# Optimization experiments

Measured on AMD Instinct MI355X. Metric: run time of the kernel, lower is better.

## Reference

```python
import jax, jax.numpy as jnp
import numpy as np

E = 524288
B = 16
NODE_IN = 128
EDGE_IN = 64
GLOBAL_IN = 64
HIDDEN = 256
EDGE_OUT = 64
CAT_IN = EDGE_IN + 2 * NODE_IN + GLOBAL_IN  # 384


def setup_inputs() -> dict:
    key = jax.random.key(0)
    ks = jax.random.split(key, 9)
    src = jax.random.normal(ks[0], (E, NODE_IN), dtype=jnp.float32)
    dest = jax.random.normal(ks[1], (E, NODE_IN), dtype=jnp.float32)
    edge_attr = jax.random.normal(ks[2], (E, EDGE_IN), dtype=jnp.float32)
    u = jax.random.normal(ks[3], (B, GLOBAL_IN), dtype=jnp.float32)
    batch = jnp.sort(jax.random.randint(ks[4], (E,), 0, B, dtype=jnp.int64))
    # MLP params (torch Linear default init scale ~1/sqrt(fan_in))
    W1 = jax.random.normal(ks[5], (CAT_IN, HIDDEN), dtype=jnp.float32) / np.sqrt(CAT_IN)
    b1 = jax.random.normal(ks[6], (HIDDEN,), dtype=jnp.float32) / np.sqrt(CAT_IN)
    W2 = jax.random.normal(ks[7], (HIDDEN, EDGE_OUT), dtype=jnp.float32) / np.sqrt(HIDDEN)
    b2 = jax.random.normal(ks[8], (EDGE_OUT,), dtype=jnp.float32) / np.sqrt(HIDDEN)
    return {"src": src, "dest": dest, "edge_attr": edge_attr, "u": u,
            "batch": batch, "W1": W1, "b1": b1, "W2": W2, "b2": b2}


def reference(src, dest, edge_attr, u, batch, W1, b1, W2, b2):
    # gather global features per edge, concat, 2-layer MLP with ReLU
    x = jnp.concatenate([src, dest, edge_attr, u[batch]], axis=1)  # [E, 384]
    h = jax.nn.relu(x @ W1 + b1)                                   # [E, hidden]
    return h @ W2 + b2                                             # [E, edge_out]
```

## Files before the change

### kernel.cpp

```cpp
#include <hip/hip_runtime.h>

typedef __bf16 bf16_t;
typedef bf16_t bf16x8 __attribute__((ext_vector_type(8)));
typedef float f32x4 __attribute__((ext_vector_type(4)));
typedef unsigned short u16;
typedef unsigned int u32;

#define E_TOT 524288
#define MT 64
#define NBLK (E_TOT / MT)

__device__ __forceinline__ u16 f2bf(float f) {
  u32 u = __builtin_bit_cast(u32, f);
  u += 0x7FFFu + ((u >> 16) & 1u);
  return (u16)(u >> 16);
}

__device__ __forceinline__ bf16x8 pack8(f32x4 a, f32x4 b) {
  bf16x8 p;
  p[0] = (bf16_t)a[0]; p[1] = (bf16_t)a[1]; p[2] = (bf16_t)a[2]; p[3] = (bf16_t)a[3];
  p[4] = (bf16_t)b[0]; p[5] = (bf16_t)b[1]; p[6] = (bf16_t)b[2]; p[7] = (bf16_t)b[3];
  return p;
}

__device__ __forceinline__ void gload_lds16(const void* g, void* l) {
  __builtin_amdgcn_global_load_lds(
      (const __attribute__((address_space(1))) u32*)g,
      (__attribute__((address_space(3))) u32*)l, 16, 0, 0);
}

__global__ void prep_w1tc(const float* __restrict__ W1, u16* __restrict__ W1Tc) {
  int t = blockIdx.x * 256 + threadIdx.x;
  if (t < 384 * 256) {
    int U = t >> 3, e = t & 7;
    int c = U >> 10, rem = U & 1023;
    int n = rem >> 2, j = rem & 3;
    int k = c * 32 + ((j ^ ((n >> 1) & 3)) << 3) + e;
    W1Tc[t] = f2bf(W1[k * 256 + n]);
  }
}

__global__ void prep_w2t(const float* __restrict__ W2, u16* __restrict__ W2T) {
  int t = blockIdx.x * 256 + threadIdx.x;
  if (t < 64 * 256) {
    int n = t / 256, k = t % 256;
    W2T[t] = f2bf(W2[k * 64 + n]);
  }
}

__global__ void __launch_bounds__(256) edge_fused(
    const float* __restrict__ src, const float* __restrict__ dst,
    const float* __restrict__ ea, const float* __restrict__ u,
    const int* __restrict__ batch, const u16* __restrict__ W1Tc,
    const float* __restrict__ b1, const u16* __restrict__ W2T,
    const float* __restrict__ b2, float* __restrict__ out)
{
  __shared__ __align__(16) u16 smem[20480];
  u16* As = smem;
  u16* Wb = smem + 4096;
  u16* Hs = smem;

  const int t    = threadIdx.x;
  const int wid  = t >> 6;
  const int lane = t & 63;
  const int lr   = lane & 15;
  const int lg   = lane >> 4;
  const int e0   = blockIdx.x * MT;
  const int r    = t >> 2;
  const int jcol = t & 3;
  const int bidx = batch[e0 + r];
  const int wunit = r * 4 + (jcol ^ ((r >> 1) & 3));

  auto loadA = [&](int c, f32x4* ra) {
    const float* p;
    if (c < 4)       p = src + (size_t)(e0 + r) * 128 + c * 32 + jcol * 8;
    else if (c < 8)  p = dst + (size_t)(e0 + r) * 128 + (c - 4) * 32 + jcol * 8;
    else if (c < 10) p = ea + (size_t)(e0 + r) * 64 + (c - 8) * 32 + jcol * 8;
    else             p = u + (size_t)bidx * 64 + (c - 10) * 32 + jcol * 8;
    ra[0] = *(const f32x4*)p;
    ra[1] = *(const f32x4*)(p + 4);
  };
  auto issueW = [&](int c, u16* Wn) {
    #pragma unroll
    for (int g = 0; g < 4; ++g) {
      int ub = wid * 256 + g * 64;
      gload_lds16(W1Tc + ((size_t)c * 1024 + ub + lane) * 8, Wn + ub * 8);
    }
  };

  f32x4 ra[2], rb[2];
  loadA(0, ra);
  issueW(0, Wb);
  loadA(1, rb);
  issueW(1, Wb + 8192);

  f32x4 acc[4][4];
  #pragma unroll
  for (int i = 0; i < 4; ++i)
    #pragma unroll
    for (int j = 0; j < 4; ++j)
      acc[i][j] = (f32x4){0.f, 0.f, 0.f, 0.f};

  #pragma unroll
  for (int kb = 0; kb < 12; ++kb) {
    f32x4* rc = (kb & 1) ? rb : ra;
    u16* Ab = As + (kb & 1) * 2048;
    u16* Wc = Wb + (kb & 1) * 8192;

    *(bf16x8*)&Ab[wunit * 8] = pack8(rc[0], rc[1]);
    if (kb <= 9) loadA(kb + 2, rc);

    if (kb <= 9)      asm volatile("s_waitcnt vmcnt(8) lgkmcnt(0)" ::: "memory");
    else if (kb == 10) asm volatile("s_waitcnt vmcnt(6) lgkmcnt(0)" ::: "memory");
    else               asm volatile("s_waitcnt vmcnt(0) lgkmcnt(0)" ::: "memory");
    __builtin_amdgcn_sched_barrier(0);
    __builtin_amdgcn_s_barrier();

    __builtin_amdgcn_s_setprio(1);
    bf16x8 af[4];
    #pragma unroll
    for (int mf = 0; mf < 4; ++mf) {
      int row = mf * 16 + lr;
      af[mf] = *(const bf16x8*)&Ab[(row * 4 + (lg ^ ((row >> 1) & 3))) * 8];
    }
    #pragma unroll
    for (int nf = 0; nf < 4; ++nf) {
      int n = wid * 64 + nf * 16 + lr;
      bf16x8 bfr = *(const bf16x8*)&Wc[(n * 4 + (lg ^ ((n >> 1) & 3))) * 8];
      #pragma unroll
      for (int mf = 0; mf < 4; ++mf)
        acc[mf][nf] = __builtin_amdgcn_mfma_f32_16x16x32_bf16(af[mf], bfr, acc[mf][nf], 0, 0, 0);
    }
    __builtin_amdgcn_s_setprio(0);
    __builtin_amdgcn_s_barrier();

    if (kb <= 9) issueW(kb + 2, Wc);
  }

  float bias1[4];
  #pragma unroll
  for (int nf = 0; nf < 4; ++nf) bias1[nf] = b1[wid * 64 + nf * 16 + lr];
  #pragma unroll
  for (int mf = 0; mf < 4; ++mf)
    #pragma unroll
    for (int nf = 0; nf < 4; ++nf)
      #pragma unroll
      for (int rr = 0; rr < 4; ++rr) {
        int row = mf * 16 + lg * 4 + rr;
        int col = wid * 64 + nf * 16 + lr;
        float v = fmaxf(acc[mf][nf][rr] + bias1[nf], 0.f);
        Hs[row * 256 + ((((col >> 3) ^ (row & 7)) << 3) | (col & 7))] = f2bf(v);
      }
  __syncthreads();

  const int n2 = wid * 16 + lr;
  bf16x8 b2f[8];
  #pragma unroll
  for (int ks = 0; ks < 8; ++ks)
    b2f[ks] = *(const bf16x8*)(W2T + n2 * 256 + ks * 32 + lg * 8);
  const float bb = b2[n2];

  f32x4 acc2[4];
  #pragma unroll
  for (int mf = 0; mf < 4; ++mf) acc2[mf] = (f32x4){0.f, 0.f, 0.f, 0.f};
  #pragma unroll
  for (int ks = 0; ks < 8; ++ks) {
    #pragma unroll
    for (int mf = 0; mf < 4; ++mf) {
      int row = mf * 16 + lr;
      bf16x8 a = *(const bf16x8*)&Hs[row * 256 + (((ks * 4 + lg) ^ (row & 7)) << 3)];
      acc2[mf] = __builtin_amdgcn_mfma_f32_16x16x32_bf16(a, b2f[ks], acc2[mf], 0, 0, 0);
    }
  }

  #pragma unroll
  for (int mf = 0; mf < 4; ++mf)
    #pragma unroll
    for (int rr = 0; rr < 4; ++rr) {
      int row = e0 + mf * 16 + lg * 4 + rr;
      out[(size_t)row * 64 + n2] = acc2[mf][rr] + bb;
    }
}

extern "C" void kernel_launch(void* const* d_in, const int* in_sizes, int n_in,
                              void* d_out, int out_size, void* d_ws, size_t ws_size,
                              hipStream_t stream) {
  const float* src  = (const float*)d_in[0];
  const float* dst  = (const float*)d_in[1];
  const float* ea   = (const float*)d_in[2];
  const float* u    = (const float*)d_in[3];
  const int* batch  = (const int*)d_in[4];
  const float* W1   = (const float*)d_in[5];
  const float* b1   = (const float*)d_in[6];
  const float* W2   = (const float*)d_in[7];
  const float* b2   = (const float*)d_in[8];
  float* out = (float*)d_out;

  u16* W1Tc = (u16*)d_ws;
  u16* W2T  = W1Tc + 384 * 256;

  prep_w1tc<<<(384 * 256 + 255) / 256, 256, 0, stream>>>(W1, W1Tc);
  prep_w2t<<<(64 * 256 + 255) / 256, 256, 0, stream>>>(W2, W2T);
  edge_fused<<<NBLK, 256, 0, stream>>>(src, dst, ea, u, batch, W1Tc, b1, W2T, b2, out);
}
```

Baseline: 235.2 us.

## Load W1 fragments directly to registers and transpose MFMA operand roles

Weights are now pre-packed into per-lane MFMA fragment order so each wave loads its W1 B-fragments straight from global/L2 into registers, removing the LDS staging buffer for W1 and one barrier per k-step. The MFMA operands are swapped so the accumulator layout gives each lane contiguous columns, enabling vectorized bias loads, bf16x4 LDS stores of the hidden layer, and f32x4 output stores instead of scalar stores. This cuts LDS footprint and barrier count but relies on L2 for repeated weight reads per block and raises VGPR pressure from double-buffered weight fragments.

Result: no change. 234.7 us (-0.2%).

```diff
diff --git a/kernel.cpp b/kernel.cpp
--- a/kernel.cpp
+++ b/kernel.cpp
@@ -2,6 +2,7 @@
 
 typedef __bf16 bf16_t;
 typedef bf16_t bf16x8 __attribute__((ext_vector_type(8)));
+typedef bf16_t bf16x4 __attribute__((ext_vector_type(4)));
 typedef float f32x4 __attribute__((ext_vector_type(4)));
 typedef unsigned short u16;
 typedef unsigned int u32;
@@ -23,41 +24,42 @@
   return p;
 }
 
-__device__ __forceinline__ void gload_lds16(const void* g, void* l) {
-  __builtin_amdgcn_global_load_lds(
-      (const __attribute__((address_space(1))) u32*)g,
-      (__attribute__((address_space(3))) u32*)l, 16, 0, 0);
-}
-
-__global__ void prep_w1tc(const float* __restrict__ W1, u16* __restrict__ W1Tc) {
+__global__ void prep_w1f(const float* __restrict__ W1, u16* __restrict__ W1F) {
   int t = blockIdx.x * 256 + threadIdx.x;
-  if (t < 384 * 256) {
-    int U = t >> 3, e = t & 7;
-    int c = U >> 10, rem = U & 1023;
-    int n = rem >> 2, j = rem & 3;
-    int k = c * 32 + ((j ^ ((n >> 1) & 3)) << 3) + e;
-    W1Tc[t] = f2bf(W1[k * 256 + n]);
+  if (t < 98304) {
+    int e  = t & 7;
+    int l  = (t >> 3) & 63;
+    int nf = (t >> 9) & 3;
+    int wc = (t >> 11) & 3;
+    int kb = t >> 13;
+    int n = wc * 64 + nf * 16 + (l & 15);
+    int k = kb * 32 + ((l >> 4) << 3) + e;
+    W1F[t] = f2bf(W1[k * 256 + n]);
   }
 }
 
-__global__ void prep_w2t(const float* __restrict__ W2, u16* __restrict__ W2T) {
+__global__ void prep_w2f(const float* __restrict__ W2, u16* __restrict__ W2F) {
   int t = blockIdx.x * 256 + threadIdx.x;
-  if (t < 64 * 256) {
-    int n = t / 256, k = t % 256;
-    W2T[t] = f2bf(W2[k * 64 + n]);
+  if (t < 16384) {
+    int e   = t & 7;
+    int l   = (t >> 3) & 63;
+    int n2f = (t >> 9) & 3;
+    int ks  = t >> 11;
+    int n2 = n2f * 16 + (l & 15);
+    int k  = ks * 32 + ((l >> 4) << 3) + e;
+    W2F[t] = f2bf(W2[k * 64 + n2]);
   }
 }
 
 __global__ void __launch_bounds__(256) edge_fused(
     const float* __restrict__ src, const float* __restrict__ dst,
     const float* __restrict__ ea, const float* __restrict__ u,
-    const int* __restrict__ batch, const u16* __restrict__ W1Tc,
-    const float* __restrict__ b1, const u16* __restrict__ W2T,
+    const int* __restrict__ batch, const u16* __restrict__ W1F,
+    const float* __restrict__ b1, const u16* __restrict__ W2F,
     const float* __restrict__ b2, float* __restrict__ out)
 {
-  __shared__ __align__(16) u16 smem[20480];
+  __shared__ __align__(16) u16 smem[16384];
   u16* As = smem;
-  u16* Wb = smem + 4096;
   u16* Hs = smem;
 
   const int t    = threadIdx.x;
@@ -80,19 +82,20 @@
     ra[0] = *(const f32x4*)p;
     ra[1] = *(const f32x4*)(p + 4);
   };
-  auto issueW = [&](int c, u16* Wn) {
-    #pragma unroll
-    for (int g = 0; g < 4; ++g) {
-      int ub = wid * 256 + g * 64;
-      gload_lds16(W1Tc + ((size_t)c * 1024 + ub + lane) * 8, Wn + ub * 8);
-    }
+  auto loadW1 = [&](int c, bf16x8* wf) {
+    const u16* p = W1F + ((size_t)(c * 4 + wid) * 4) * 512 + lane * 8;
+    wf[0] = *(const bf16x8*)(p);
+    wf[1] = *(const bf16x8*)(p + 512);
+    wf[2] = *(const bf16x8*)(p + 1024);
+    wf[3] = *(const bf16x8*)(p + 1536);
   };
 
   f32x4 ra[2], rb[2];
+  bf16x8 wA[4], wB[4];
   loadA(0, ra);
-  issueW(0, Wb);
+  loadW1(0, wA);
   loadA(1, rb);
-  issueW(1, Wb + 8192);
+  loadW1(1, wB);
 
   f32x4 acc[4][4];
   #pragma unroll
@@ -103,18 +106,13 @@
 
   #pragma unroll
   for (int kb = 0; kb < 12; ++kb) {
-    f32x4* rc = (kb & 1) ? rb : ra;
+    f32x4*  rc = (kb & 1) ? rb : ra;
+    bf16x8* wc_ = (kb & 1) ? wB : wA;
     u16* Ab = As + (kb & 1) * 2048;
-    u16* Wc = Wb + (kb & 1) * 8192;
 
     *(bf16x8*)&Ab[wunit * 8] = pack8(rc[0], rc[1]);
     if (kb <= 9) loadA(kb + 2, rc);
-
-    if (kb <= 9)      asm volatile("s_waitcnt vmcnt(8) lgkmcnt(0)" ::: "memory");
-    else if (kb == 10) asm volatile("s_waitcnt vmcnt(6) lgkmcnt(0)" ::: "memory");
-    else               asm volatile("s_waitcnt vmcnt(0) lgkmcnt(0)" ::: "memory");
-    __builtin_amdgcn_sched_barrier(0);
-    __builtin_amdgcn_s_barrier();
+    __syncthreads();
 
     __builtin_amdgcn_s_setprio(1);
     bf16x8 af[4];
@@ -124,62 +122,55 @@
       af[mf] = *(const bf16x8*)&Ab[(row * 4 + (lg ^ ((row >> 1) & 3))) * 8];
     }
     #pragma unroll
-    for (int nf = 0; nf < 4; ++nf) {
-      int n = wid * 64 + nf * 16 + lr;
-      bf16x8 bfr = *(const bf16x8*)&Wc[(n * 4 + (lg ^ ((n >> 1) & 3))) * 8];
+    for (int nf = 0; nf < 4; ++nf)
       #pragma unroll
       for (int mf = 0; mf < 4; ++mf)
-        acc[mf][nf] = __builtin_amdgcn_mfma_f32_16x16x32_bf16(af[mf], bfr, acc[mf][nf], 0, 0, 0);
-    }
+        acc[nf][mf] = __builtin_amdgcn_mfma_f32_16x16x32_bf16(wc_[nf], af[mf], acc[nf][mf], 0, 0, 0);
     __builtin_amdgcn_s_setprio(0);
-    __builtin_amdgcn_s_barrier();
 
-    if (kb <= 9) issueW(kb + 2, Wc);
+    if (kb <= 9) loadW1(kb + 2, wc_);
   }
-
-  float bias1[4];
-  #pragma unroll
-  for (int nf = 0; nf < 4; ++nf) bias1[nf] = b1[wid * 64 + nf * 16 + lr];
-  #pragma unroll
-  for (int mf = 0; mf < 4; ++mf)
-    #pragma unroll
-    for (int nf = 0; nf < 4; ++nf)
-      #pragma unroll
-      for (int rr = 0; rr < 4; ++rr) {
-        int row = mf * 16 + lg * 4 + rr;
-        int col = wid * 64 + nf * 16 + lr;
-        float v = fmaxf(acc[mf][nf][rr] + bias1[nf], 0.f);
-        Hs[row * 256 + ((((col >> 3) ^ (row & 7)) << 3) | (col & 7))] = f2bf(v);
-      }
   __syncthreads();
 
-  const int n2 = wid * 16 + lr;
-  bf16x8 b2f[8];
   #pragma unroll
-  for (int ks = 0; ks < 8; ++ks)
-    b2f[ks] = *(const bf16x8*)(W2T + n2 * 256 + ks * 32 + lg * 8);
-  const float bb = b2[n2];
-
-  f32x4 acc2[4];
-  #pragma unroll
-  for (int mf = 0; mf < 4; ++mf) acc2[mf] = (f32x4){0.f, 0.f, 0.f, 0.f};
-  #pragma unroll
-  for (int ks = 0; ks < 8; ++ks) {
+  for (int nf = 0; nf < 4; ++nf) {
+    f32x4 b1v = *(const f32x4*)(b1 + wid * 64 + nf * 16 + lg * 4);
     #pragma unroll
     for (int mf = 0; mf < 4; ++mf) {
       int row = mf * 16 + lr;
-      bf16x8 a = *(const bf16x8*)&Hs[row * 256 + (((ks * 4 + lg) ^ (row & 7)) << 3)];
-      acc2[mf] = __builtin_amdgcn_mfma_f32_16x16x32_bf16(a, b2f[ks], acc2[mf], 0, 0, 0);
+      bf16x4 hb;
+      #pragma unroll
+      for (int rr = 0; rr < 4; ++rr)
+        hb[rr] = (bf16_t)fmaxf(acc[nf][mf][rr] + b1v[rr], 0.f);
+      int uu = (wid * 4 + nf) * 4 + lg;
+      int up = uu ^ ((row & 3) << 3);
+      *(bf16x4*)&Hs[row * 256 + up * 4] = hb;
     }
+  }
+  __syncthreads();
+
+  const int row2 = wid * 16 + lr;
+  f32x4 d2[4];
+  #pragma unroll
+  for (int i = 0; i < 4; ++i) d2[i] = (f32x4){0.f, 0.f, 0.f, 0.f};
+  #pragma unroll
+  for (int ks = 0; ks < 8; ++ks) {
+    int uu = ks * 8 + lg * 2;
+    int up = uu ^ ((row2 & 3) << 3);
+    bf16x8 a2 = *(const bf16x8*)&Hs[row2 * 256 + up * 4];
+    const u16* q = W2F + (size_t)ks * 2048 + lane * 8;
+    #pragma unroll
+    for (int n2f = 0; n2f < 4; ++n2f)
+      d2[n2f] = __builtin_amdgcn_mfma_f32_16x16x32_bf16(
+          *(const bf16x8*)(q + n2f * 512), a2, d2[n2f], 0, 0, 0);
   }
 
   #pragma unroll
-  for (int mf = 0; mf < 4; ++mf)
-    #pragma unroll
-    for (int rr = 0; rr < 4; ++rr) {
-      int row = e0 + mf * 16 + lg * 4 + rr;
-      out[(size_t)row * 64 + n2] = acc2[mf][rr] + bb;
-    }
+  for (int n2f = 0; n2f < 4; ++n2f) {
+    f32x4 b2v = *(const f32x4*)(b2 + n2f * 16 + lg * 4);
+    f32x4 ov = d2[n2f] + b2v;
+    *(f32x4*)&out[(size_t)(e0 + row2) * 64 + n2f * 16 + lg * 4] = ov;
+  }
 }
 
 extern "C" void kernel_launch(void* const* d_in, const int* in_sizes, int n_in,
@@ -196,10 +187,10 @@
   const float* b2   = (const float*)d_in[8];
   float* out = (float*)d_out;
 
-  u16* W1Tc = (u16*)d_ws;
-  u16* W2T  = W1Tc + 384 * 256;
+  u16* W1F = (u16*)d_ws;
+  u16* W2F = W1F + 98304;
 
-  prep_w1tc<<<(384 * 256 + 255) / 256, 256, 0, stream>>>(W1, W1Tc);
-  prep_w2t<<<(64 * 256 + 255) / 256, 256, 0, stream>>>(W2, W2T);
-  edge_fused<<<NBLK, 256, 0, stream>>>(src, dst, ea, u, batch, W1Tc, b1, W2T, b2, out);
+  prep_w1f<<<384, 256, 0, stream>>>(W1, W1F);
+  prep_w2f<<<64, 256, 0, stream>>>(W2, W2F);
+  edge_fused<<<NBLK, 256, 0, stream>>>(src, dst, ea, u, batch, W1F, b1, W2F, b2, out);
 }
```
